# Optimization experiments

Hardware: AMD Instinct MI355X
Metric: run time of the kernel (lower is better)

Reference implementation:

```python
import jax, jax.numpy as jnp
import numpy as np

SEQ_LEN, BATCH, INPUT_SIZE, HIDDEN_SIZE = 2048, 64, 512, 512


def _xavier_uniform(key, shape, dtype=jnp.float32):
    fan_out, fan_in = shape
    limit = float(np.sqrt(6.0 / (fan_in + fan_out)))
    return jax.random.uniform(key, shape, dtype, -limit, limit)


def setup_inputs() -> dict:
    key = jax.random.key(0)
    kx, kh, kW, kU, kb1, kb2 = jax.random.split(key, 6)
    x = jax.random.normal(kx, (SEQ_LEN, BATCH, INPUT_SIZE), dtype=jnp.float32)
    prev_hidden = jax.random.normal(kh, (BATCH, HIDDEN_SIZE), dtype=jnp.float32)
    W = _xavier_uniform(kW, (HIDDEN_SIZE, INPUT_SIZE))
    U = _xavier_uniform(kU, (HIDDEN_SIZE, HIDDEN_SIZE))
    # torch nn.init.uniform_ default is U(0, 1)
    hidden_bias = jax.random.uniform(kb1, (HIDDEN_SIZE,), dtype=jnp.float32)
    input_bias = jax.random.uniform(kb2, (HIDDEN_SIZE,), dtype=jnp.float32)
    return {"x": x, "prev_hidden": prev_hidden, "W": W, "U": U,
            "hidden_bias": hidden_bias, "input_bias": input_bias}


def reference(x, prev_hidden, W, U, hidden_bias, input_bias):
    # Faithful to the source: the loop never updates `prev_hidden`, so the
    # recurrent term U @ h0 + b_h is CONSTANT across timesteps and each
    # output is out_t = tanh(W x_t + b_in + U h0 + b_h). This vectorizes
    # into one batched GEMM over all timesteps plus a broadcast add.
    # x: (T, B, I); W: (H, I); U: (H, H)
    wx = jnp.einsum('tbi,hi->tbh', x, W) + input_bias          # (T, B, H)
    uh = prev_hidden @ U.T + hidden_bias                        # (B, H)
    outputs = jnp.tanh(wx + uh[None, :, :])                     # (T, B, H)
    hidden = outputs[-1]                                        # (B, H)
    return outputs, hidden
```

## Files before the change

### kernel.cpp

```cpp
#include <hip/hip_runtime.h>
#include <hip/hip_bf16.h>
#include <cstdint>
#include <cstddef>


#define T_LEN 2048
#define BATCH 64
#define ISZ 512
#define HSZ 512
#define MTOT (T_LEN * BATCH)

#define BM 128
#define BN 128
#define NMT (MTOT / BM)

typedef __attribute__((ext_vector_type(8))) __bf16 bf16x8;
typedef __attribute__((ext_vector_type(4))) __bf16 bf16x4;
typedef __attribute__((ext_vector_type(4))) float f32x4;

#define GLOBAL_AS __attribute__((address_space(1)))
#define LDS_AS __attribute__((address_space(3)))

__device__ __forceinline__ float fast_tanh(float v) {
    float e = __expf(2.0f * v);
    return 1.0f - 2.0f / (e + 1.0f);
}

__global__ __launch_bounds__(512) void prep_kernel(const float* __restrict__ W,
                                                   __bf16* __restrict__ Wbf,
                                                   const float* __restrict__ prev,
                                                   const float* __restrict__ U,
                                                   const float* __restrict__ hb,
                                                   const float* __restrict__ ib,
                                                   float* __restrict__ uh) {
    if (blockIdx.x < 128) {
        int i = blockIdx.x * 512 + threadIdx.x;
        f32x4 f = ((const f32x4*)W)[i];
        bf16x4 v;
        v[0] = (__bf16)f[0]; v[1] = (__bf16)f[1];
        v[2] = (__bf16)f[2]; v[3] = (__bf16)f[3];
        ((bf16x4*)Wbf)[i] = v;
    } else {
        __shared__ float sp[HSZ];
        int b = blockIdx.x - 128, h = threadIdx.x;
        sp[h] = prev[b * HSZ + h];
        __syncthreads();
        const float* urow = U + (size_t)h * HSZ;
        float acc = 0.f;
#pragma unroll 4
        for (int i = 0; i < HSZ; i += 4) {
            f32x4 u4 = *(const f32x4*)(urow + i);
            acc += u4[0] * sp[i] + u4[1] * sp[i + 1] + u4[2] * sp[i + 2] + u4[3] * sp[i + 3];
        }
        uh[b * HSZ + h] = acc + hb[h] + ib[h];
    }
}

__global__ __launch_bounds__(256, 3) void gemm_tanh_kernel(
        const float* __restrict__ x, const __bf16* __restrict__ Wbf,
        const float* __restrict__ uh, float* __restrict__ out,
        float* __restrict__ hid) {
    __shared__ __attribute__((aligned(16))) char lds[2][24576];

    int orig = blockIdx.x;
    int wg = (orig & 7) * 512 + (orig >> 3);
    int mt = wg >> 2, nt = wg & 3;

    int tid = threadIdx.x;
    int lane = tid & 63, wid = tid >> 6;
    int wr = wid >> 1, wc = wid & 1;
    int l15 = lane & 15, l4 = lane >> 4;

    const size_t m0 = (size_t)mt * BM;
    const int n0 = nt * BN;

    int a_r = lane >> 3, a_s = lane & 7;
    const float* aSrc[4];
#pragma unroll
    for (int j = 0; j < 4; ++j) {
        int c = wid * 4 + j;
        aSrc[j] = x + (m0 + c * 8 + a_r) * ISZ + ((a_s ^ a_r) << 2);
    }
    int b_r = lane >> 2, b_s = lane & 3, b_x = (lane >> 3) & 3;
    const __bf16* bSrc[2];
#pragma unroll
    for (int j = 0; j < 2; ++j) {
        int c = wid * 2 + j;
        bSrc[j] = Wbf + (size_t)(n0 + c * 16 + b_r) * ISZ + ((b_s ^ b_x) << 3);
    }

    auto stage = [&](int buf, int ks) {
        char* base = lds[buf];
#pragma unroll
        for (int j = 0; j < 4; ++j)
            __builtin_amdgcn_global_load_lds(
                (const GLOBAL_AS uint32_t*)(aSrc[j] + ks),
                (LDS_AS uint32_t*)(base + (wid * 4 + j) * 1024), 16, 0, 0);
#pragma unroll
        for (int j = 0; j < 2; ++j)
            __builtin_amdgcn_global_load_lds(
                (const GLOBAL_AS uint32_t*)(bSrc[j] + ks),
                (LDS_AS uint32_t*)(base + 16384 + (wid * 2 + j) * 1024), 16, 0, 0);
    };

    f32x4 acc[4][4] = {};

    auto compute = [&](int buf) {
        const char* base = lds[buf];
        bf16x8 bfr[4];
#pragma unroll
        for (int ni = 0; ni < 4; ++ni) {
            int row = wc * 64 + ni * 16 + l15;
            bfr[ni] = *(const bf16x8*)(base + 16384 + row * 64 +
                                       ((l4 * 16) ^ (((row >> 1) & 3) << 4)));
        }
#pragma unroll
        for (int mi = 0; mi < 4; ++mi) {
            int row = wr * 64 + mi * 16 + l15;
            int xo = (row & 7) << 4;
            f32x4 a0 = *(const f32x4*)(base + row * 128 + ((l4 * 32) ^ xo));
            f32x4 a1 = *(const f32x4*)(base + row * 128 + ((l4 * 32 + 16) ^ xo));
            bf16x8 av;
            av[0] = (__bf16)a0[0]; av[1] = (__bf16)a0[1];
            av[2] = (__bf16)a0[2]; av[3] = (__bf16)a0[3];
            av[4] = (__bf16)a1[0]; av[5] = (__bf16)a1[1];
            av[6] = (__bf16)a1[2]; av[7] = (__bf16)a1[3];
#pragma unroll
            for (int ni = 0; ni < 4; ++ni)
                acc[mi][ni] = __builtin_amdgcn_mfma_f32_16x16x32_bf16(
                    bfr[ni], av, acc[mi][ni], 0, 0, 0);
        }
    };

    stage(0, 0);
    __syncthreads();

    int cur = 0;
#pragma unroll 1
    for (int t = 0; t < 16; ++t) {
        if (t < 15) stage(cur ^ 1, (t + 1) * 32);
        compute(cur);
        if (t < 15) __syncthreads();
        cur ^= 1;
    }

    bool lastTile = (mt == NMT - 1);
#pragma unroll
    for (int mi = 0; mi < 4; ++mi) {
        int ml = wr * 64 + mi * 16 + l15;
        size_t m = m0 + ml;
        int bb = ml & 63;
#pragma unroll
        for (int ni = 0; ni < 4; ++ni) {
            int nb = n0 + wc * 64 + ni * 16 + l4 * 4;
            f32x4 u4 = *(const f32x4*)&uh[bb * HSZ + nb];
            f32x4 v;
#pragma unroll
            for (int r = 0; r < 4; ++r) v[r] = fast_tanh(acc[mi][ni][r] + u4[r]);
            *(f32x4*)&out[m * HSZ + nb] = v;
            if (lastTile && ml >= BM - BATCH)
                *(f32x4*)&hid[(size_t)(ml - (BM - BATCH)) * HSZ + nb] = v;
        }
    }
}

extern "C" void kernel_launch(void* const* d_in, const int* in_sizes, int n_in,
                              void* d_out, int out_size, void* d_ws, size_t ws_size,
                              hipStream_t stream) {
    const float* x  = (const float*)d_in[0];
    const float* ph = (const float*)d_in[1];
    const float* W  = (const float*)d_in[2];
    const float* U  = (const float*)d_in[3];
    const float* hb = (const float*)d_in[4];
    const float* ib = (const float*)d_in[5];
    float* out = (float*)d_out;
    float* hid = out + (size_t)MTOT * HSZ;

    __bf16* Wbf = (__bf16*)d_ws;
    float* uh   = (float*)((char*)d_ws + 512 * 1024);

    hipLaunchKernelGGL(prep_kernel, dim3(192), dim3(512), 0, stream,
                       W, Wbf, ph, U, hb, ib, uh);
    hipLaunchKernelGGL(gemm_tanh_kernel, dim3(4096), dim3(256), 0, stream,
                       x, Wbf, uh, out, hid);
}
```

Before: 254.6 us.

## Triple-buffer LDS staging with partial vmcnt waits in GEMM-tanh loop

Moves the GEMM main loop from double to triple buffering, keeping two K-slices in flight. Each iteration waits with a partial vmcnt (6 outstanding loads) instead of a full drain, then issues one barrier per step, so global-to-LDS loads overlap compute more deeply. LDS per block grows from 48KB to 72KB and the occupancy hint of 3 is dropped, which may cut the number of resident workgroups per CU. Correctness depends on the vmcnt count matching the six loads issued per stage and on the barrier ordering before buffers are reused.

```diff
diff --git a/kernel.cpp b/kernel.cpp
--- a/kernel.cpp
+++ b/kernel.cpp
@@ -56,11 +56,11 @@
     }
 }
 
-__global__ __launch_bounds__(256, 3) void gemm_tanh_kernel(
+__global__ __launch_bounds__(256) void gemm_tanh_kernel(
         const float* __restrict__ x, const __bf16* __restrict__ Wbf,
         const float* __restrict__ uh, float* __restrict__ out,
         float* __restrict__ hid) {
-    __shared__ __attribute__((aligned(16))) char lds[2][24576];
+    __shared__ __attribute__((aligned(16))) char lds[3][24576];
 
     int orig = blockIdx.x;
     int wg = (orig & 7) * 512 + (orig >> 3);
@@ -89,8 +89,8 @@
         bSrc[j] = Wbf + (size_t)(n0 + c * 16 + b_r) * ISZ + ((b_s ^ b_x) << 3);
     }
 
-    auto stage = [&](int buf, int ks) {
-        char* base = lds[buf];
+    auto stage = [&](char* base, int t) {
+        int ks = t * 32;
 #pragma unroll
         for (int j = 0; j < 4; ++j)
             __builtin_amdgcn_global_load_lds(
@@ -105,8 +105,7 @@
 
     f32x4 acc[4][4] = {};
 
-    auto compute = [&](int buf) {
-        const char* base = lds[buf];
+    auto compute = [&](const char* base) {
         bf16x8 bfr[4];
 #pragma unroll
         for (int ni = 0; ni < 4; ++ni) {
@@ -132,17 +131,24 @@
         }
     };
 
-    stage(0, 0);
-    __syncthreads();
+    stage(lds[0], 0);
+    stage(lds[1], 1);
 
-    int cur = 0;
 #pragma unroll 1
-    for (int t = 0; t < 16; ++t) {
-        if (t < 15) stage(cur ^ 1, (t + 1) * 32);
-        compute(cur);
-        if (t < 15) __syncthreads();
-        cur ^= 1;
+    for (int t = 0; t < 15; ++t) {
+        asm volatile("s_waitcnt vmcnt(6)" ::: "memory");
+        __builtin_amdgcn_sched_barrier(0);
+        __builtin_amdgcn_s_barrier();
+        __builtin_amdgcn_sched_barrier(0);
+        int nxt = t + 2;
+        if (nxt < 16) stage(lds[nxt % 3], nxt);
+        compute(lds[t % 3]);
     }
+    asm volatile("s_waitcnt vmcnt(0)" ::: "memory");
+    __builtin_amdgcn_sched_barrier(0);
+    __builtin_amdgcn_s_barrier();
+    __builtin_amdgcn_sched_barrier(0);
+    compute(lds[0]);
 
     bool lastTile = (mt == NMT - 1);
 #pragma unroll
```

After: 276.2 us. +8.5%, slower.
